# Kernel tuning notes

Hardware: AMD Instinct MI355X
Metric: run time of the kernel (lower is better)

The kernel has to match this reference:

```python
import jax, jax.numpy as jnp
import numpy as np

N_NODES = 100000
N_EDGES = 3200000
N_GRAPHS = 512
F_IN = 256
HID = 16
N_CLS = 8


def setup_inputs() -> dict:
    key = jax.random.key(0)
    ks = jax.random.split(key, 6)
    x = jax.random.normal(ks[0], (N_NODES, F_IN), jnp.float32)
    edge_index = jax.random.randint(ks[1], (2, N_EDGES), 0, N_NODES, dtype=jnp.int64)
    batch = jnp.sort(jax.random.randint(ks[2], (N_NODES,), 0, N_GRAPHS, dtype=jnp.int64))
    W1 = jax.random.normal(ks[3], (F_IN, HID), jnp.float32) / np.float32(np.sqrt(F_IN))
    b1 = jnp.zeros((HID,), jnp.float32)
    W2 = jax.random.normal(ks[4], (HID, N_CLS), jnp.float32) / np.float32(np.sqrt(HID))
    b2 = jnp.zeros((N_CLS,), jnp.float32)
    return {"x": x, "edge_index": edge_index, "batch": batch, "num_graphs": N_GRAPHS,
            "W1": W1, "b1": b1, "W2": W2, "b2": b2}


def _gcn_conv(x, src, dst, W, b, n):
    # PyG GCNConv: linear transform, then sym-normalized scatter-add (self-loops
    # already appended to src/dst by caller), bias added after aggregation.
    h = x @ W  # [N, out]
    deg = jax.ops.segment_sum(jnp.ones_like(dst, h.dtype), dst, num_segments=n)
    dinv = jax.lax.rsqrt(jnp.maximum(deg, 1.0))  # deg >= 1 due to self-loops
    norm = dinv[src] * dinv[dst]  # [E+N]
    out = jax.ops.segment_sum(h[src] * norm[:, None], dst, num_segments=n)
    return out + b


def reference(x, edge_index, batch, num_graphs, W1, b1, W2, b2):
    n = x.shape[0]
    loop = jnp.arange(n, dtype=edge_index.dtype)
    src = jnp.concatenate([edge_index[0], loop])
    dst = jnp.concatenate([edge_index[1], loop])
    h = jax.nn.relu(_gcn_conv(x, src, dst, W1, b1, n))
    h = _gcn_conv(h, src, dst, W2, b2, n)
    # global mean pool over graphs
    sums = jax.ops.segment_sum(h, batch, num_segments=num_graphs)
    cnt = jax.ops.segment_sum(jnp.ones((n,), h.dtype), batch, num_segments=num_graphs)
    return sums / jnp.maximum(cnt, 1.0)[:, None]
```

## Files before the change

kernel.cpp:

```cpp
#include <hip/hip_runtime.h>

#define F_IN 256
#define HID 16
#define NCLS 8
#define BSH 9
#define NPB 512
#define MAXBINS 256
#define BCAP 18432u
#define TILE 8192
#define WIN 8
#define GROWS 64
#define APITCH 280

typedef float f4v __attribute__((ext_vector_type(4)));
typedef float f32x4 __attribute__((ext_vector_type(4)));
typedef _Float16 h2v __attribute__((ext_vector_type(2)));
typedef _Float16 f16x4 __attribute__((ext_vector_type(4)));
typedef _Float16 f16x8 __attribute__((ext_vector_type(8)));

__global__ void k_init(unsigned* __restrict__ binCur, int nbins,
                       const float* __restrict__ W1, _Float16* __restrict__ wfrag,
                       float* __restrict__ cg, int g,
                       float* __restrict__ out, int osz) {
    int t = threadIdx.x;
    if (t < nbins) binCur[t] = (unsigned)t * BCAP;
    if (t < 64) {
        int col = t & 15, k0 = (t >> 4) * 8;
#pragma unroll
        for (int kc = 0; kc < 8; ++kc) {
            f16x8 v;
#pragma unroll
            for (int j = 0; j < 8; ++j)
                v[j] = (_Float16)W1[(kc * 32 + k0 + j) * HID + col];
            *(f16x8*)&wfrag[((size_t)t * 8 + kc) * 8] = v;
        }
    }
    for (int i = t; i < g; i += 256) cg[i] = 0.f;
    for (int i = t; i < osz; i += 256) out[i] = 0.f;
}

__global__ void __launch_bounds__(512) k_binA(const int* __restrict__ src,
                                              const int* __restrict__ dst, int e,
                                              unsigned* __restrict__ binCur,
                                              unsigned* __restrict__ binbuf) {
    __shared__ unsigned scnt[MAXBINS], lbase[MAXBINS], gbase[MAXBINS];
    __shared__ unsigned sbuf[TILE];
    __shared__ unsigned char sbin[TILE];
    int t = threadIdx.x;
    if (t < MAXBINS) scnt[t] = 0u;
    __syncthreads();
    int base = blockIdx.x * TILE;
    unsigned ent[16], rank[16];
    int ebin[16];
#pragma unroll
    for (int i = 0; i < 16; ++i) {
        int j = base + t + i * 512;
        ebin[i] = -1;
        if (j < e) {
            int d = __builtin_nontemporal_load(&dst[j]);
            int s = __builtin_nontemporal_load(&src[j]);
            ent[i] = ((unsigned)s << BSH) | ((unsigned)d & (NPB - 1));
            ebin[i] = d >> BSH;
            rank[i] = atomicAdd(&scnt[ebin[i]], 1u);
        }
    }
    __syncthreads();
    if (t == 0) {
        unsigned run = 0;
        for (int b = 0; b < MAXBINS; ++b) { lbase[b] = run; run += scnt[b]; }
    }
    __syncthreads();
    if (t < MAXBINS && scnt[t] > 0u) gbase[t] = atomicAdd(&binCur[t], scnt[t]);
    __syncthreads();
#pragma unroll
    for (int i = 0; i < 16; ++i)
        if (ebin[i] >= 0) {
            unsigned p = lbase[ebin[i]] + rank[i];
            sbuf[p] = ent[i];
            sbin[p] = (unsigned char)ebin[i];
        }
    __syncthreads();
    int total = e - base; if (total > TILE) total = TILE;
    for (int idx = t; idx < total; idx += 512) {
        int b = sbin[idx];
        __builtin_nontemporal_store(sbuf[idx], &binbuf[gbase[b] + ((unsigned)idx - lbase[b])]);
    }
}

__global__ void __launch_bounds__(256) k_binB(const unsigned* __restrict__ binbuf,
                                              const unsigned* __restrict__ binCur,
                                              int n,
                                              unsigned* __restrict__ srcs,
                                              unsigned* __restrict__ off,
                                              unsigned* __restrict__ degc) {
    __shared__ unsigned hist[NPB];
    __shared__ unsigned pref[NPB];
    __shared__ unsigned s1[256];
    int t = threadIdx.x;
    int b = blockIdx.x;
    unsigned base = (unsigned)b * BCAP;
    unsigned end = binCur[b];
    for (int i = t; i < NPB; i += 256) hist[i] = 0u;
    __syncthreads();
    for (unsigned j = base + t; j < end; j += 256)
        atomicAdd(&hist[__builtin_nontemporal_load(&binbuf[j]) & (NPB - 1)], 1u);
    __syncthreads();
    unsigned h0 = hist[2 * t], h1 = hist[2 * t + 1];
    unsigned pair = h0 + h1;
    s1[t] = pair;
    __syncthreads();
    for (int o = 1; o < 256; o <<= 1) {
        unsigned v = (t >= o) ? s1[t - o] : 0u;
        __syncthreads();
        s1[t] += v;
        __syncthreads();
    }
    unsigned exc = s1[t] - pair;
    pref[2 * t] = exc;
    pref[2 * t + 1] = exc + h0;
    __syncthreads();
    int dbase = b << BSH;
    for (int i = t; i < NPB; i += 256) {
        int d = dbase + i;
        if (d < n) { off[d] = base + pref[i]; degc[d] = hist[i]; }
    }
    __syncthreads();
    for (int i = t; i < NPB; i += 256) hist[i] = 0u;
    __syncthreads();
    for (unsigned j = base + t; j < end; j += 256) {
        unsigned v = __builtin_nontemporal_load(&binbuf[j]);
        unsigned dl = v & (NPB - 1);
        unsigned r = atomicAdd(&hist[dl], 1u);
        srcs[base + pref[dl] + r] = v >> BSH;
    }
}

__global__ void __launch_bounds__(256) k_gemm1(const float* __restrict__ x,
                                               const _Float16* __restrict__ wfrag,
                                               const unsigned* __restrict__ degc,
                                               _Float16* __restrict__ t1h, int n) {
    __shared__ _Float16 xs[4][16 * APITCH];
    int t = threadIdx.x;
    int lane = t & 63;
    int wv = t >> 6;
    int col = lane & 15;
    int k0 = (lane >> 4) * 8;
    f16x8 bfrag[8];
#pragma unroll
    for (int kc = 0; kc < 8; ++kc)
        bfrag[kc] = *(const f16x8*)&wfrag[((size_t)lane * 8 + kc) * 8];
    int rbase = blockIdx.x * GROWS;
    int nrows = n - rbase; if (nrows > GROWS) nrows = GROWS;
#pragma unroll
    for (int it = 0; it < GROWS * 64 / 256; ++it) {
        int q = t + it * 256;
        int row = q >> 6, c4 = q & 63;
        if (row < nrows) {
            f4v v = __builtin_nontemporal_load(
                &((const f4v*)(x + (size_t)(rbase + row) * F_IN))[c4]);
            f16x4 hv;
            hv[0] = (_Float16)v[0]; hv[1] = (_Float16)v[1];
            hv[2] = (_Float16)v[2]; hv[3] = (_Float16)v[3];
            *(f16x4*)&xs[row >> 4][(row & 15) * APITCH + c4 * 4] = hv;
        }
    }
    __syncthreads();
    f32x4 acc = {0.f, 0.f, 0.f, 0.f};
    const _Float16* tile = xs[wv];
    int arow = lane & 15;
#pragma unroll
    for (int kc = 0; kc < 8; ++kc) {
        f16x8 afrag = *(const f16x8*)&tile[arow * APITCH + kc * 32 + k0];
        acc = __builtin_amdgcn_mfma_f32_16x16x32_f16(afrag, bfrag[kc], acc, 0, 0, 0);
    }
    int r0 = (lane >> 4) * 4;
#pragma unroll
    for (int reg = 0; reg < 4; ++reg) {
        int grow = rbase + wv * 16 + r0 + reg;
        if (grow < n) {
            float v = acc[reg] * rsqrtf((float)(degc[grow] + 1u));
            t1h[(size_t)grow * HID + col] = (_Float16)v;
        }
    }
}

__global__ void __launch_bounds__(256) k_agg1g2(const unsigned* __restrict__ srcs,
                                                const unsigned* __restrict__ off,
                                                const unsigned* __restrict__ degc,
                                                const unsigned* __restrict__ t1h,
                                                const float* __restrict__ b1,
                                                const float* __restrict__ W2,
                                                unsigned* __restrict__ t2h, int n) {
    __shared__ float w2s[HID * NCLS];
    __shared__ float b1s[HID];
    int t = threadIdx.x;
    if (t < HID * NCLS) w2s[t] = W2[t];
    if (t < HID) b1s[t] = b1[t];
    __syncthreads();
    int d = blockIdx.x * 16 + (t >> 4);
    if (d >= n) return;
    int lane8 = t & 7;
    int oct = (t >> 3) & 1;
    unsigned p = off[d];
    unsigned c = degc[d];
    float a0 = 0.f, a1 = 0.f;
    union { unsigned u; h2v h; } cv;
    unsigned i = oct;
    for (; i + 6 < c; i += 8) {
        unsigned s0 = srcs[p + i],     s1 = srcs[p + i + 2];
        unsigned s2 = srcs[p + i + 4], s3 = srcs[p + i + 6];
        unsigned w0 = t1h[(size_t)s0 * 8 + lane8];
        unsigned w1 = t1h[(size_t)s1 * 8 + lane8];
        unsigned w2 = t1h[(size_t)s2 * 8 + lane8];
        unsigned w3 = t1h[(size_t)s3 * 8 + lane8];
        cv.u = w0; a0 += (float)cv.h[0]; a1 += (float)cv.h[1];
        cv.u = w1; a0 += (float)cv.h[0]; a1 += (float)cv.h[1];
        cv.u = w2; a0 += (float)cv.h[0]; a1 += (float)cv.h[1];
        cv.u = w3; a0 += (float)cv.h[0]; a1 += (float)cv.h[1];
    }
    for (; i + 2 < c; i += 4) {
        unsigned s0 = srcs[p + i], s1 = srcs[p + i + 2];
        unsigned w0 = t1h[(size_t)s0 * 8 + lane8];
        unsigned w1 = t1h[(size_t)s1 * 8 + lane8];
        cv.u = w0; a0 += (float)cv.h[0]; a1 += (float)cv.h[1];
        cv.u = w1; a0 += (float)cv.h[0]; a1 += (float)cv.h[1];
    }
    if (i < c) {
        unsigned w = t1h[(size_t)srcs[p + i] * 8 + lane8];
        cv.u = w; a0 += (float)cv.h[0]; a1 += (float)cv.h[1];
    }
    a0 += __shfl_xor(a0, 8, 64);
    a1 += __shfl_xor(a1, 8, 64);
    if (oct != 0) return;
    cv.u = t1h[(size_t)d * 8 + lane8];
    a0 += (float)cv.h[0]; a1 += (float)cv.h[1];
    float di = rsqrtf((float)(c + 1u));
    float h0 = fmaxf(di * a0 + b1s[2 * lane8], 0.f);
    float h1 = fmaxf(di * a1 + b1s[2 * lane8 + 1], 0.f);
    float o[NCLS];
#pragma unroll
    for (int cc = 0; cc < NCLS; ++cc)
        o[cc] = h0 * w2s[(2 * lane8) * NCLS + cc] + h1 * w2s[(2 * lane8 + 1) * NCLS + cc];
#pragma unroll
    for (int m = 1; m < 8; m <<= 1)
#pragma unroll
        for (int cc = 0; cc < NCLS; ++cc)
            o[cc] += __shfl_xor(o[cc], m, 64);
    if (lane8 < 4) {
        union { unsigned u; h2v h; } pk;
        pk.h[0] = (_Float16)(o[2 * lane8] * di);
        pk.h[1] = (_Float16)(o[2 * lane8 + 1] * di);
        t2h[(size_t)d * 4 + lane8] = pk.u;
    }
}

__global__ void __launch_bounds__(256) k_agg2pool(const unsigned* __restrict__ srcs,
                                                  const unsigned* __restrict__ off,
                                                  const unsigned* __restrict__ degc,
                                                  const unsigned* __restrict__ t2h,
                                                  const float* __restrict__ b2,
                                                  const int* __restrict__ batch,
                                                  float* __restrict__ out,
                                                  float* __restrict__ cg, int n) {
    __shared__ float wacc[WIN * NCLS];
    __shared__ float wcnt[WIN];
    __shared__ int gb_s;
    int t = threadIdx.x;
    int bbase = blockIdx.x * 32;
    if (t < WIN * NCLS) wacc[t] = 0.f;
    if (t < WIN) wcnt[t] = 0.f;
    if (t == 0) gb_s = batch[bbase < n ? bbase : (n - 1)];
    __syncthreads();
    int d = bbase + (t >> 3);
    int lane4 = t & 3;
    int pr = (t >> 2) & 1;
    if (d < n) {
        unsigned p = off[d];
        unsigned c = degc[d];
        float a0 = 0.f, a1 = 0.f;
        union { unsigned u; h2v h; } cv;
        unsigned i = pr;
        for (; i + 6 < c; i += 8) {
            unsigned w0 = t2h[(size_t)srcs[p + i] * 4 + lane4];
            unsigned w1 = t2h[(size_t)srcs[p + i + 2] * 4 + lane4];
            unsigned w2 = t2h[(size_t)srcs[p + i + 4] * 4 + lane4];
            unsigned w3 = t2h[(size_t)srcs[p + i + 6] * 4 + lane4];
            cv.u = w0; a0 += (float)cv.h[0]; a1 += (float)cv.h[1];
            cv.u = w1; a0 += (float)cv.h[0]; a1 += (float)cv.h[1];
            cv.u = w2; a0 += (float)cv.h[0]; a1 += (float)cv.h[1];
            cv.u = w3; a0 += (float)cv.h[0]; a1 += (float)cv.h[1];
        }
        for (; i + 2 < c; i += 4) {
            unsigned w0 = t2h[(size_t)srcs[p + i] * 4 + lane4];
            unsigned w1 = t2h[(size_t)srcs[p + i + 2] * 4 + lane4];
            cv.u = w0; a0 += (float)cv.h[0]; a1 += (float)cv.h[1];
            cv.u = w1; a0 += (float)cv.h[0]; a1 += (float)cv.h[1];
        }
        if (i < c) {
            unsigned w = t2h[(size_t)srcs[p + i] * 4 + lane4];
            cv.u = w; a0 += (float)cv.h[0]; a1 += (float)cv.h[1];
        }
        a0 += __shfl_xor(a0, 4, 64);
        a1 += __shfl_xor(a1, 4, 64);
        if (pr == 0) {
            cv.u = t2h[(size_t)d * 4 + lane4];
            a0 += (float)cv.h[0]; a1 += (float)cv.h[1];
            float di = rsqrtf((float)(c + 1u));
            float v0 = di * a0 + b2[2 * lane4];
            float v1 = di * a1 + b2[2 * lane4 + 1];
            int g = batch[d];
            int gi = g - gb_s;
            if (gi < WIN) {
                atomicAdd(&wacc[gi * NCLS + 2 * lane4], v0);
                atomicAdd(&wacc[gi * NCLS + 2 * lane4 + 1], v1);
                if ((t & 7) == 0) atomicAdd(&wcnt[gi], 1.f);
            } else {
                atomicAdd(&out[(size_t)g * NCLS + 2 * lane4], v0);
                atomicAdd(&out[(size_t)g * NCLS + 2 * lane4 + 1], v1);
                if ((t & 7) == 0) atomicAdd(&cg[g], 1.f);
            }
        }
    }
    __syncthreads();
    if (t < WIN * NCLS && wcnt[t >> 3] > 0.f)
        atomicAdd(&out[(size_t)(gb_s + (t >> 3)) * NCLS + (t & 7)], wacc[t]);
    if (t < WIN && wcnt[t] > 0.f) atomicAdd(&cg[gb_s + t], wcnt[t]);
}

__global__ void k_div(float* __restrict__ out, const float* __restrict__ cg, int total) {
    int i = blockIdx.x * blockDim.x + threadIdx.x;
    if (i < total) out[i] /= fmaxf(cg[i / NCLS], 1.0f);
}

extern "C" void kernel_launch(void* const* d_in, const int* in_sizes, int n_in,
                              void* d_out, int out_size, void* d_ws, size_t ws_size,
                              hipStream_t stream) {
    const float* x = (const float*)d_in[0];
    const int* ei = (const int*)d_in[1];
    const int* batch = (const int*)d_in[2];
    const float* W1 = (const float*)d_in[4];
    const float* b1 = (const float*)d_in[5];
    const float* W2 = (const float*)d_in[6];
    const float* b2 = (const float*)d_in[7];

    int n = in_sizes[0] / F_IN;
    int e = in_sizes[1] / 2;
    int g = out_size / NCLS;
    const int* src = ei;
    const int* dst = ei + e;
    int nbins = (n + NPB - 1) >> BSH;

    char* w = (char*)d_ws;
    unsigned* binCur = (unsigned*)w; w += (size_t)MAXBINS * 4;
    unsigned* degc   = (unsigned*)w; w += (size_t)n * 4;
    unsigned* off    = (unsigned*)w; w += (size_t)n * 4;
    unsigned* t1h    = (unsigned*)w; w += (size_t)n * 8 * 4;
    unsigned* t2h    = (unsigned*)w; w += (size_t)n * 4 * 4;
    _Float16* wfrag  = (_Float16*)w; w += (size_t)64 * 8 * 8 * 2;
    float* cg        = (float*)w;    w += (size_t)g * 4;
    w = (char*)(((size_t)w + 255) & ~(size_t)255);
    unsigned* binbuf = (unsigned*)w; w += (size_t)nbins * BCAP * 4;
    unsigned* srcs   = (unsigned*)w; w += (size_t)nbins * BCAP * 4;

    k_init<<<1, 256, 0, stream>>>(binCur, nbins, W1, wfrag, cg, g, (float*)d_out, out_size);
    k_binA<<<(e + TILE - 1) / TILE, 512, 0, stream>>>(src, dst, e, binCur, binbuf);
    k_binB<<<nbins, 256, 0, stream>>>(binbuf, binCur, n, srcs, off, degc);
    k_gemm1<<<(n + GROWS - 1) / GROWS, 256, 0, stream>>>(x, wfrag, degc, (_Float16*)t1h, n);
    k_agg1g2<<<(n + 15) / 16, 256, 0, stream>>>(srcs, off, degc, t1h, b1, W2, t2h, n);
    k_agg2pool<<<(n + 31) / 32, 256, 0, stream>>>(srcs, off, degc, t2h, b2, batch,
                                                  (float*)d_out, cg, n);
    k_div<<<(out_size + 255) / 256, 256, 0, stream>>>((float*)d_out, cg, out_size);
}
```

Measured before the change: 184.0 us.

## Widen gather loads to 16-byte vectors and stage bins in LDS

The two aggregation kernels now gather each neighbor row with 16-byte vector loads. Agg1 uses 4 threads per node instead of 16, and agg2 uses 2 instead of 8. Deeper unrolling keeps more loads in flight, and the pooling path does 8 atomics per thread instead of 2. Separately, k_binB caches its bin in LDS on the first pass so the second pass reads from LDS instead of reloading global memory. The cost is more registers per thread, fewer threads per node for high-degree nodes, and 72KB of LDS per binB block, which lowers occupancy.

```diff
diff --git a/kernel.cpp b/kernel.cpp
--- a/kernel.cpp
+++ b/kernel.cpp
@@ -14,6 +14,8 @@
 
 typedef float f4v __attribute__((ext_vector_type(4)));
 typedef float f32x4 __attribute__((ext_vector_type(4)));
+typedef unsigned u4v __attribute__((ext_vector_type(4)));
+typedef unsigned u2v __attribute__((ext_vector_type(2)));
 typedef _Float16 h2v __attribute__((ext_vector_type(2)));
 typedef _Float16 f16x4 __attribute__((ext_vector_type(4)));
 typedef _Float16 f16x8 __attribute__((ext_vector_type(8)));
@@ -93,17 +95,21 @@
                                               unsigned* __restrict__ srcs,
                                               unsigned* __restrict__ off,
                                               unsigned* __restrict__ degc) {
+    __shared__ unsigned sbuf[BCAP];
     __shared__ unsigned hist[NPB];
     __shared__ unsigned pref[NPB];
     __shared__ unsigned s1[256];
     int t = threadIdx.x;
     int b = blockIdx.x;
     unsigned base = (unsigned)b * BCAP;
-    unsigned end = binCur[b];
+    unsigned cnt = binCur[b] - base;
     for (int i = t; i < NPB; i += 256) hist[i] = 0u;
     __syncthreads();
-    for (unsigned j = base + t; j < end; j += 256)
-        atomicAdd(&hist[__builtin_nontemporal_load(&binbuf[j]) & (NPB - 1)], 1u);
+    for (unsigned j = t; j < cnt; j += 256) {
+        unsigned v = __builtin_nontemporal_load(&binbuf[base + j]);
+        sbuf[j] = v;
+        atomicAdd(&hist[v & (NPB - 1)], 1u);
+    }
     __syncthreads();
     unsigned h0 = hist[2 * t], h1 = hist[2 * t + 1];
     unsigned pair = h0 + h1;
@@ -127,8 +133,8 @@
     __syncthreads();
     for (int i = t; i < NPB; i += 256) hist[i] = 0u;
     __syncthreads();
-    for (unsigned j = base + t; j < end; j += 256) {
-        unsigned v = __builtin_nontemporal_load(&binbuf[j]);
+    for (unsigned j = t; j < cnt; j += 256) {
+        unsigned v = sbuf[j];
         unsigned dl = v & (NPB - 1);
         unsigned r = atomicAdd(&hist[dl], 1u);
         srcs[base + pref[dl] + r] = v >> BSH;
@@ -184,10 +190,15 @@
     }
 }
 
+#define ACC8(V) { cv.u = (V)[0]; a0 += (float)cv.h[0]; a1 += (float)cv.h[1]; \
+                  cv.u = (V)[1]; a2 += (float)cv.h[0]; a3 += (float)cv.h[1]; \
+                  cv.u = (V)[2]; a4 += (float)cv.h[0]; a5 += (float)cv.h[1]; \
+                  cv.u = (V)[3]; a6 += (float)cv.h[0]; a7 += (float)cv.h[1]; }
+
 __global__ void __launch_bounds__(256) k_agg1g2(const unsigned* __restrict__ srcs,
                                                 const unsigned* __restrict__ off,
                                                 const unsigned* __restrict__ degc,
-                                                const unsigned* __restrict__ t1h,
+                                                const u4v* __restrict__ t1x,
                                                 const float* __restrict__ b1,
                                                 const float* __restrict__ W2,
                                                 unsigned* __restrict__ t2h, int n) {
@@ -197,67 +208,89 @@
     if (t < HID * NCLS) w2s[t] = W2[t];
     if (t < HID) b1s[t] = b1[t];
     __syncthreads();
-    int d = blockIdx.x * 16 + (t >> 4);
+    int d = blockIdx.x * 64 + (t >> 2);
     if (d >= n) return;
-    int lane8 = t & 7;
-    int oct = (t >> 3) & 1;
+    int half = t & 1;
+    int pr = (t >> 1) & 1;
     unsigned p = off[d];
     unsigned c = degc[d];
-    float a0 = 0.f, a1 = 0.f;
+    float a0 = 0.f, a1 = 0.f, a2 = 0.f, a3 = 0.f;
+    float a4 = 0.f, a5 = 0.f, a6 = 0.f, a7 = 0.f;
     union { unsigned u; h2v h; } cv;
-    unsigned i = oct;
+    unsigned i = pr;
+    for (; i + 14 < c; i += 16) {
+        u4v w0 = t1x[(size_t)srcs[p + i] * 2 + half];
+        u4v w1 = t1x[(size_t)srcs[p + i + 2] * 2 + half];
+        u4v w2 = t1x[(size_t)srcs[p + i + 4] * 2 + half];
+        u4v w3 = t1x[(size_t)srcs[p + i + 6] * 2 + half];
+        u4v w4 = t1x[(size_t)srcs[p + i + 8] * 2 + half];
+        u4v w5 = t1x[(size_t)srcs[p + i + 10] * 2 + half];
+        u4v w6 = t1x[(size_t)srcs[p + i + 12] * 2 + half];
+        u4v w7 = t1x[(size_t)srcs[p + i + 14] * 2 + half];
+        ACC8(w0) ACC8(w1) ACC8(w2) ACC8(w3)
+        ACC8(w4) ACC8(w5) ACC8(w6) ACC8(w7)
+    }
     for (; i + 6 < c; i += 8) {
-        unsigned s0 = srcs[p + i],     s1 = srcs[p + i + 2];
-        unsigned s2 = srcs[p + i + 4], s3 = srcs[p + i + 6];
-        unsigned w0 = t1h[(size_t)s0 * 8 + lane8];
-        unsigned w1 = t1h[(size_t)s1 * 8 + lane8];
-        unsigned w2 = t1h[(size_t)s2 * 8 + lane8];
-        unsigned w3 = t1h[(size_t)s3 * 8 + lane8];
-        cv.u = w0; a0 += (float)cv.h[0]; a1 += (float)cv.h[1];
-        cv.u = w1; a0 += (float)cv.h[0]; a1 += (float)cv.h[1];
-        cv.u = w2; a0 += (float)cv.h[0]; a1 += (float)cv.h[1];
-        cv.u = w3; a0 += (float)cv.h[0]; a1 += (float)cv.h[1];
+        u4v w0 = t1x[(size_t)srcs[p + i] * 2 + half];
+        u4v w1 = t1x[(size_t)srcs[p + i + 2] * 2 + half];
+        u4v w2 = t1x[(size_t)srcs[p + i + 4] * 2 + half];
+        u4v w3 = t1x[(size_t)srcs[p + i + 6] * 2 + half];
+        ACC8(w0) ACC8(w1) ACC8(w2) ACC8(w3)
     }
     for (; i + 2 < c; i += 4) {
-        unsigned s0 = srcs[p + i], s1 = srcs[p + i + 2];
-        unsigned w0 = t1h[(size_t)s0 * 8 + lane8];
-        unsigned w1 = t1h[(size_t)s1 * 8 + lane8];
-        cv.u = w0; a0 += (float)cv.h[0]; a1 += (float)cv.h[1];
-        cv.u = w1; a0 += (float)cv.h[0]; a1 += (float)cv.h[1];
+        u4v w0 = t1x[(size_t)srcs[p + i] * 2 + half];
+        u4v w1 = t1x[(size_t)srcs[p + i + 2] * 2 + half];
+        ACC8(w0) ACC8(w1)
     }
     if (i < c) {
-        unsigned w = t1h[(size_t)srcs[p + i] * 8 + lane8];
-        cv.u = w; a0 += (float)cv.h[0]; a1 += (float)cv.h[1];
-    }
-    a0 += __shfl_xor(a0, 8, 64);
-    a1 += __shfl_xor(a1, 8, 64);
-    if (oct != 0) return;
-    cv.u = t1h[(size_t)d * 8 + lane8];
-    a0 += (float)cv.h[0]; a1 += (float)cv.h[1];
+        u4v w0 = t1x[(size_t)srcs[p + i] * 2 + half];
+        ACC8(w0)
+    }
+    a0 += __shfl_xor(a0, 2, 64);
+    a1 += __shfl_xor(a1, 2, 64);
+    a2 += __shfl_xor(a2, 2, 64);
+    a3 += __shfl_xor(a3, 2, 64);
+    a4 += __shfl_xor(a4, 2, 64);
+    a5 += __shfl_xor(a5, 2, 64);
+    a6 += __shfl_xor(a6, 2, 64);
+    a7 += __shfl_xor(a7, 2, 64);
+    u4v sl = t1x[(size_t)d * 2 + half];
+    ACC8(sl)
     float di = rsqrtf((float)(c + 1u));
-    float h0 = fmaxf(di * a0 + b1s[2 * lane8], 0.f);
-    float h1 = fmaxf(di * a1 + b1s[2 * lane8 + 1], 0.f);
+    int k0 = 8 * half;
+    float h[8];
+    h[0] = fmaxf(di * a0 + b1s[k0 + 0], 0.f);
+    h[1] = fmaxf(di * a1 + b1s[k0 + 1], 0.f);
+    h[2] = fmaxf(di * a2 + b1s[k0 + 2], 0.f);
+    h[3] = fmaxf(di * a3 + b1s[k0 + 3], 0.f);
+    h[4] = fmaxf(di * a4 + b1s[k0 + 4], 0.f);
+    h[5] = fmaxf(di * a5 + b1s[k0 + 5], 0.f);
+    h[6] = fmaxf(di * a6 + b1s[k0 + 6], 0.f);
+    h[7] = fmaxf(di * a7 + b1s[k0 + 7], 0.f);
     float o[NCLS];
 #pragma unroll
-    for (int cc = 0; cc < NCLS; ++cc)
-        o[cc] = h0 * w2s[(2 * lane8) * NCLS + cc] + h1 * w2s[(2 * lane8 + 1) * NCLS + cc];
-#pragma unroll
-    for (int m = 1; m < 8; m <<= 1)
-#pragma unroll
-        for (int cc = 0; cc < NCLS; ++cc)
-            o[cc] += __shfl_xor(o[cc], m, 64);
-    if (lane8 < 4) {
-        union { unsigned u; h2v h; } pk;
-        pk.h[0] = (_Float16)(o[2 * lane8] * di);
-        pk.h[1] = (_Float16)(o[2 * lane8 + 1] * di);
-        t2h[(size_t)d * 4 + lane8] = pk.u;
+    for (int cc = 0; cc < NCLS; ++cc) {
+        float s = 0.f;
+#pragma unroll
+        for (int j = 0; j < 8; ++j) s += h[j] * w2s[(k0 + j) * NCLS + cc];
+        o[cc] = s;
+    }
+#pragma unroll
+    for (int cc = 0; cc < NCLS; ++cc) o[cc] += __shfl_xor(o[cc], 1, 64);
+    if (pr == 0) {
+        int f0 = 4 * half;
+        union { unsigned u; h2v h; } pa, pb;
+        pa.h[0] = (_Float16)(o[f0 + 0] * di); pa.h[1] = (_Float16)(o[f0 + 1] * di);
+        pb.h[0] = (_Float16)(o[f0 + 2] * di); pb.h[1] = (_Float16)(o[f0 + 3] * di);
+        u2v pk; pk[0] = pa.u; pk[1] = pb.u;
+        *(u2v*)&t2h[(size_t)d * 4 + half * 2] = pk;
     }
 }
 
 __global__ void __launch_bounds__(256) k_agg2pool(const unsigned* __restrict__ srcs,
                                                   const unsigned* __restrict__ off,
                                                   const unsigned* __restrict__ degc,
-                                                  const unsigned* __restrict__ t2h,
+                                                  const u4v* __restrict__ t2x,
                                                   const float* __restrict__ b2,
                                                   const int* __restrict__ batch,
                                                   float* __restrict__ out,
@@ -266,58 +299,73 @@
     __shared__ float wcnt[WIN];
     __shared__ int gb_s;
     int t = threadIdx.x;
-    int bbase = blockIdx.x * 32;
+    int bbase = blockIdx.x * 128;
     if (t < WIN * NCLS) wacc[t] = 0.f;
     if (t < WIN) wcnt[t] = 0.f;
     if (t == 0) gb_s = batch[bbase < n ? bbase : (n - 1)];
     __syncthreads();
-    int d = bbase + (t >> 3);
-    int lane4 = t & 3;
-    int pr = (t >> 2) & 1;
+    int d = bbase + (t >> 1);
+    int pr = t & 1;
     if (d < n) {
         unsigned p = off[d];
         unsigned c = degc[d];
-        float a0 = 0.f, a1 = 0.f;
+        float a0 = 0.f, a1 = 0.f, a2 = 0.f, a3 = 0.f;
+        float a4 = 0.f, a5 = 0.f, a6 = 0.f, a7 = 0.f;
         union { unsigned u; h2v h; } cv;
         unsigned i = pr;
+        for (; i + 14 < c; i += 16) {
+            u4v w0 = t2x[srcs[p + i]];
+            u4v w1 = t2x[srcs[p + i + 2]];
+            u4v w2 = t2x[srcs[p + i + 4]];
+            u4v w3 = t2x[srcs[p + i + 6]];
+            u4v w4 = t2x[srcs[p + i + 8]];
+            u4v w5 = t2x[srcs[p + i + 10]];
+            u4v w6 = t2x[srcs[p + i + 12]];
+            u4v w7 = t2x[srcs[p + i + 14]];
+            ACC8(w0) ACC8(w1) ACC8(w2) ACC8(w3)
+            ACC8(w4) ACC8(w5) ACC8(w6) ACC8(w7)
+        }
         for (; i + 6 < c; i += 8) {
-            unsigned w0 = t2h[(size_t)srcs[p + i] * 4 + lane4];
-            unsigned w1 = t2h[(size_t)srcs[p + i + 2] * 4 + lane4];
-            unsigned w2 = t2h[(size_t)srcs[p + i + 4] * 4 + lane4];
-            unsigned w3 = t2h[(size_t)srcs[p + i + 6] * 4 + lane4];
-            cv.u = w0; a0 += (float)cv.h[0]; a1 += (float)cv.h[1];
-            cv.u = w1; a0 += (float)cv.h[0]; a1 += (float)cv.h[1];
-            cv.u = w2; a0 += (float)cv.h[0]; a1 += (float)cv.h[1];
-            cv.u = w3; a0 += (float)cv.h[0]; a1 += (float)cv.h[1];
+            u4v w0 = t2x[srcs[p + i]];
+            u4v w1 = t2x[srcs[p + i + 2]];
+            u4v w2 = t2x[srcs[p + i + 4]];
+            u4v w3 = t2x[srcs[p + i + 6]];
+            ACC8(w0) ACC8(w1) ACC8(w2) ACC8(w3)
         }
         for (; i + 2 < c; i += 4) {
-            unsigned w0 = t2h[(size_t)srcs[p + i] * 4 + lane4];
-            unsigned w1 = t2h[(size_t)srcs[p + i + 2] * 4 + lane4];
-            cv.u = w0; a0 += (float)cv.h[0]; a1 += (float)cv.h[1];
-            cv.u = w1; a0 += (float)cv.h[0]; a1 += (float)cv.h[1];
+            u4v w0 = t2x[srcs[p + i]];
+            u4v w1 = t2x[srcs[p + i + 2]];
+            ACC8(w0) ACC8(w1)
         }
         if (i < c) {
-            unsigned w = t2h[(size_t)srcs[p + i] * 4 + lane4];
-            cv.u = w; a0 += (float)cv.h[0]; a1 += (float)cv.h[1];
-        }
-        a0 += __shfl_xor(a0, 4, 64);
-        a1 += __shfl_xor(a1, 4, 64);
+            u4v w0 = t2x[srcs[p + i]];
+            ACC8(w0)
+        }
+        a0 += __shfl_xor(a0, 1, 64);
+        a1 += __shfl_xor(a1, 1, 64);
+        a2 += __shfl_xor(a2, 1, 64);
+        a3 += __shfl_xor(a3, 1, 64);
+        a4 += __shfl_xor(a4, 1, 64);
+        a5 += __shfl_xor(a5, 1, 64);
+        a6 += __shfl_xor(a6, 1, 64);
+        a7 += __shfl_xor(a7, 1, 64);
         if (pr == 0) {
-            cv.u = t2h[(size_t)d * 4 + lane4];
-            a0 += (float)cv.h[0]; a1 += (float)cv.h[1];
+            u4v sl = t2x[d];
+            ACC8(sl)
             float di = rsqrtf((float)(c + 1u));
-            float v0 = di * a0 + b2[2 * lane4];
-            float v1 = di * a1 + b2[2 * lane4 + 1];
+            float v[8] = {di * a0 + b2[0], di * a1 + b2[1], di * a2 + b2[2],
+                          di * a3 + b2[3], di * a4 + b2[4], di * a5 + b2[5],
+                          di * a6 + b2[6], di * a7 + b2[7]};
             int g = batch[d];
             int gi = g - gb_s;
             if (gi < WIN) {
-                atomicAdd(&wacc[gi * NCLS + 2 * lane4], v0);
-                atomicAdd(&wacc[gi * NCLS + 2 * lane4 + 1], v1);
-                if ((t & 7) == 0) atomicAdd(&wcnt[gi], 1.f);
+#pragma unroll
+                for (int f = 0; f < 8; ++f) atomicAdd(&wacc[gi * NCLS + f], v[f]);
+                atomicAdd(&wcnt[gi], 1.f);
             } else {
-                atomicAdd(&out[(size_t)g * NCLS + 2 * lane4], v0);
-                atomicAdd(&out[(size_t)g * NCLS + 2 * lane4 + 1], v1);
-                if ((t & 7) == 0) atomicAdd(&cg[g], 1.f);
+#pragma unroll
+                for (int f = 0; f < 8; ++f) atomicAdd(&out[(size_t)g * NCLS + f], v[f]);
+                atomicAdd(&cg[g], 1.f);
             }
         }
     }
@@ -354,6 +402,7 @@
     unsigned* binCur = (unsigned*)w; w += (size_t)MAXBINS * 4;
     unsigned* degc   = (unsigned*)w; w += (size_t)n * 4;
     unsigned* off    = (unsigned*)w; w += (size_t)n * 4;
+    w = (char*)(((size_t)w + 15) & ~(size_t)15);
     unsigned* t1h    = (unsigned*)w; w += (size_t)n * 8 * 4;
     unsigned* t2h    = (unsigned*)w; w += (size_t)n * 4 * 4;
     _Float16* wfrag  = (_Float16*)w; w += (size_t)64 * 8 * 8 * 2;
@@ -366,8 +415,9 @@
     k_binA<<<(e + TILE - 1) / TILE, 512, 0, stream>>>(src, dst, e, binCur, binbuf);
     k_binB<<<nbins, 256, 0, stream>>>(binbuf, binCur, n, srcs, off, degc);
     k_gemm1<<<(n + GROWS - 1) / GROWS, 256, 0, stream>>>(x, wfrag, degc, (_Float16*)t1h, n);
-    k_agg1g2<<<(n + 15) / 16, 256, 0, stream>>>(srcs, off, degc, t1h, b1, W2, t2h, n);
-    k_agg2pool<<<(n + 31) / 32, 256, 0, stream>>>(srcs, off, degc, t2h, b2, batch,
-                                                  (float*)d_out, cg, n);
+    k_agg1g2<<<(n + 63) / 64, 256, 0, stream>>>(srcs, off, degc, (const u4v*)t1h,
+                                                b1, W2, t2h, n);
+    k_agg2pool<<<(n + 127) / 128, 256, 0, stream>>>(srcs, off, degc, (const u4v*)t2h,
+                                                    b2, batch, (float*)d_out, cg, n);
     k_div<<<(out_size + 255) / 256, 256, 0, stream>>>((float*)d_out, cg, out_size);
 }
```

Result: faster. 172.7 us (-6.1%).
